# Kernel optimization log

Measured on AMD Instinct MI355X. Metric: run time of the kernel, lower is better.

The kernel has to match this reference:

```python
import jax, jax.numpy as jnp
import numpy as np

D_K = 32  # hard-coded in original module


def setup_inputs() -> dict:
    key = jax.random.key(0)
    kq, kk, kv, km = jax.random.split(key, 4)
    B, H, S, D = 4, 12, 2048, D_K
    Q = jax.random.normal(kq, (B, H, S, D), dtype=jnp.float32)
    K = jax.random.normal(kk, (B, H, S, D), dtype=jnp.float32)
    V = jax.random.normal(kv, (B, H, S, D), dtype=jnp.float32)
    attn_mask = jax.random.bernoulli(km, 0.5, (B, H, S, S))
    return {"Q": Q, "K": K, "V": V, "attn_mask": attn_mask}


def tanh_max(a):
    # (exp(a) - exp(-a)) / sum_over_keys(exp(a) + exp(-a))
    ea = jnp.exp(a)
    ena = jnp.exp(-a)
    return (ea - ena) / (ea + ena).sum(axis=-1, keepdims=True)


def reference(Q, K, V, attn_mask):
    # scores: [B,H,S,S]
    scores = jnp.einsum("bhqd,bhkd->bhqk", Q, K) / np.sqrt(D_K).astype(np.float32)
    attn = tanh_max(scores)
    # NOTE: original calls attn.masked_fill(attn_mask, 0.0) WITHOUT assignment
    # (non-in-place), so the mask has no effect. Reproduced faithfully.
    context = jnp.einsum("bhqk,bhkd->bhqd", attn, V)
    return context
```

## Files before the change

### kernel.cpp

```cpp
#include <hip/hip_runtime.h>
#include <hip/hip_bf16.h>
#include <cstdint>
#include <cstddef>


#define SLEN 2048
#define DK   32
#define NBH  48
#define NCH  64
#define PROW 36

typedef __attribute__((ext_vector_type(8))) short bf16x8;
typedef __attribute__((ext_vector_type(4))) float f32x4;
typedef const __attribute__((address_space(1))) void* gas_ptr;
typedef __attribute__((address_space(3))) void*       las_ptr;

__device__ __forceinline__ unsigned pk2(float a, float b) {
    __hip_bfloat162 h = __float22bfloat162_rn(make_float2(a, b));
    union { __hip_bfloat162 h2; unsigned u; } cv; cv.h2 = h; return cv.u;
}
__device__ __forceinline__ unsigned short f2b(float x) {
    __hip_bfloat16 h = __float2bfloat16(x);
    union { __hip_bfloat16 h; unsigned short u; } cv; cv.h = h; return cv.u;
}

__global__ __launch_bounds__(256, 3)
void attn_fused(const float* __restrict__ Q, const float* __restrict__ K,
                const float* __restrict__ V, float* __restrict__ Out) {
    __shared__ __align__(16) float          Kst[2][32 * 32];
    __shared__ __align__(16) unsigned short Vst[2][32 * PROW];

    const int tid  = threadIdx.x;
    const int lane = tid & 63;
    const int wv   = tid >> 6;
    const int quad = lane >> 4;
    const int l16  = lane & 15;

    const int b   = blockIdx.x;
    const int xcd = b & 7;
    const int i   = b >> 3;
    const int bh  = xcd * 6 + (i % 6);
    const int qblk = i / 6;
    const int qbase = qblk * 128 + wv * 32;

    const float sc = 0.17677669529663687f * 1.4426950408889634f;
    union { bf16x8 v; unsigned u[4]; } aQ0, aQ1;
    {
        const float* qp0 = Q + ((size_t)bh * SLEN + qbase + l16) * DK + quad * 8;
        float4 qa = *(const float4*)qp0;
        float4 qb = *(const float4*)(qp0 + 4);
        aQ0.u[0] = pk2(qa.x * sc, qa.y * sc); aQ0.u[1] = pk2(qa.z * sc, qa.w * sc);
        aQ0.u[2] = pk2(qb.x * sc, qb.y * sc); aQ0.u[3] = pk2(qb.z * sc, qb.w * sc);
        const float* qp1 = qp0 + 16 * DK;
        float4 qc = *(const float4*)qp1;
        float4 qd = *(const float4*)(qp1 + 4);
        aQ1.u[0] = pk2(qc.x * sc, qc.y * sc); aQ1.u[1] = pk2(qc.z * sc, qc.w * sc);
        aQ1.u[2] = pk2(qd.x * sc, qd.y * sc); aQ1.u[3] = pk2(qd.z * sc, qd.w * sc);
    }

    const float* Kh = K + (size_t)bh * SLEN * DK;
    const float* Vh = V + (size_t)bh * SLEN * DK;

    const int grow   = wv * 8 + (lane >> 3);
    const int spos   = lane & 7;
    const int schunk = spos ^ ((grow >> 1) & 7);
    const int ksrc   = grow * 32 + schunk * 4;
    const int vsrc   = grow * 32 + spos * 4;
    const int vcol   = spos * 4;

    const int rkey0 = 8 * (l16 >> 2) + 2 * (l16 & 3);
    const int rxor  = (rkey0 >> 1) & 7;
    const int rc0   = ((2 * quad + 0) ^ rxor) * 4;
    const int rc1   = ((2 * quad + 1) ^ rxor) * 4;

    f32x4 o00 = {0,0,0,0}, o01 = {0,0,0,0};
    f32x4 o10 = {0,0,0,0}, o11 = {0,0,0,0};
    float den0 = 0.f, den1 = 0.f;
    const f32x4 zero = {0,0,0,0};

    __builtin_amdgcn_global_load_lds((gas_ptr)(Kh + ksrc),
                                     (las_ptr)(&Kst[0][wv * 256]), 16, 0, 0);
    float4 vreg = *(const float4*)(Vh + vsrc);
    {
        unsigned short* vtw = &Vst[0][0];
        vtw[(vcol + 0) * PROW + grow] = f2b(vreg.x);
        vtw[(vcol + 1) * PROW + grow] = f2b(vreg.y);
        vtw[(vcol + 2) * PROW + grow] = f2b(vreg.z);
        vtw[(vcol + 3) * PROW + grow] = f2b(vreg.w);
    }
    __syncthreads();

    for (int c = 0; c < NCH; ++c) {
        const int buf = c & 1, nbuf = buf ^ 1;
        if (c + 1 < NCH) {
            __builtin_amdgcn_global_load_lds(
                (gas_ptr)(Kh + (c + 1) * 1024 + ksrc),
                (las_ptr)(&Kst[nbuf][wv * 256]), 16, 0, 0);
            vreg = *(const float4*)(Vh + (c + 1) * 1024 + vsrc);
        }

        const float* kb_ = &Kst[buf][0];
        float4 e0 = *(const float4*)(kb_ + rkey0 * 32 + rc0);
        float4 e1 = *(const float4*)(kb_ + rkey0 * 32 + rc1);
        float4 d0 = *(const float4*)(kb_ + (rkey0 + 1) * 32 + rc0);
        float4 d1 = *(const float4*)(kb_ + (rkey0 + 1) * 32 + rc1);
        union { bf16x8 v; unsigned u[4]; } kf0, kf1;
        kf0.u[0] = pk2(e0.x, e0.y); kf0.u[1] = pk2(e0.z, e0.w);
        kf0.u[2] = pk2(e1.x, e1.y); kf0.u[3] = pk2(e1.z, e1.w);
        kf1.u[0] = pk2(d0.x, d0.y); kf1.u[1] = pk2(d0.z, d0.w);
        kf1.u[2] = pk2(d1.x, d1.y); kf1.u[3] = pk2(d1.z, d1.w);

        f32x4 s00 = __builtin_amdgcn_mfma_f32_16x16x32_bf16(kf0.v, aQ0.v, zero, 0, 0, 0);
        f32x4 s01 = __builtin_amdgcn_mfma_f32_16x16x32_bf16(kf1.v, aQ0.v, zero, 0, 0, 0);
        f32x4 s10 = __builtin_amdgcn_mfma_f32_16x16x32_bf16(kf0.v, aQ1.v, zero, 0, 0, 0);
        f32x4 s11 = __builtin_amdgcn_mfma_f32_16x16x32_bf16(kf1.v, aQ1.v, zero, 0, 0, 0);

        const unsigned short* vt = &Vst[buf][0];
        union { bf16x8 v; uint2 h[2]; } V0, V1;
        {
            const unsigned short* p0 = vt + l16 * PROW + quad * 8;
            V0.h[0] = *(const uint2*)p0;
            V0.h[1] = *(const uint2*)(p0 + 4);
            const unsigned short* p1 = vt + (16 + l16) * PROW + quad * 8;
            V1.h[0] = *(const uint2*)p1;
            V1.h[1] = *(const uint2*)(p1 + 4);
        }

        union { bf16x8 v; unsigned u[4]; } aP0, aP1;
        #pragma unroll
        for (int r = 0; r < 4; ++r) {
            float e0_  = __builtin_amdgcn_exp2f(s00[r]);
            float en0_ = __builtin_amdgcn_exp2f(-s00[r]);
            float e1_  = __builtin_amdgcn_exp2f(s01[r]);
            float en1_ = __builtin_amdgcn_exp2f(-s01[r]);
            den0 += (e0_ + en0_) + (e1_ + en1_);
            aP0.u[r] = pk2(e0_ - en0_, e1_ - en1_);
        }
        #pragma unroll
        for (int r = 0; r < 4; ++r) {
            float e0_  = __builtin_amdgcn_exp2f(s10[r]);
            float en0_ = __builtin_amdgcn_exp2f(-s10[r]);
            float e1_  = __builtin_amdgcn_exp2f(s11[r]);
            float en1_ = __builtin_amdgcn_exp2f(-s11[r]);
            den1 += (e0_ + en0_) + (e1_ + en1_);
            aP1.u[r] = pk2(e0_ - en0_, e1_ - en1_);
        }

        o00 = __builtin_amdgcn_mfma_f32_16x16x32_bf16(aP0.v, V0.v, o00, 0, 0, 0);
        o01 = __builtin_amdgcn_mfma_f32_16x16x32_bf16(aP0.v, V1.v, o01, 0, 0, 0);
        o10 = __builtin_amdgcn_mfma_f32_16x16x32_bf16(aP1.v, V0.v, o10, 0, 0, 0);
        o11 = __builtin_amdgcn_mfma_f32_16x16x32_bf16(aP1.v, V1.v, o11, 0, 0, 0);

        if (c + 1 < NCH) {
            unsigned short* vtw = &Vst[nbuf][0];
            vtw[(vcol + 0) * PROW + grow] = f2b(vreg.x);
            vtw[(vcol + 1) * PROW + grow] = f2b(vreg.y);
            vtw[(vcol + 2) * PROW + grow] = f2b(vreg.z);
            vtw[(vcol + 3) * PROW + grow] = f2b(vreg.w);
        }
        __syncthreads();
    }

    den0 += __shfl_xor(den0, 16); den0 += __shfl_xor(den0, 32);
    den1 += __shfl_xor(den1, 16); den1 += __shfl_xor(den1, 32);

    float* outp = Out + ((size_t)bh * SLEN + qbase) * DK;
    #pragma unroll
    for (int rr = 0; rr < 4; ++rr) {
        float inv0 = 1.0f / __shfl(den0, quad * 4 + rr, 16);
        float inv1 = 1.0f / __shfl(den1, quad * 4 + rr, 16);
        int q0 = quad * 4 + rr;
        int q1 = 16 + quad * 4 + rr;
        outp[(size_t)q0 * DK + l16]      = o00[rr] * inv0;
        outp[(size_t)q0 * DK + 16 + l16] = o01[rr] * inv0;
        outp[(size_t)q1 * DK + l16]      = o10[rr] * inv1;
        outp[(size_t)q1 * DK + 16 + l16] = o11[rr] * inv1;
    }
}

extern "C" void kernel_launch(void* const* d_in, const int* in_sizes, int n_in,
                              void* d_out, int out_size, void* d_ws, size_t ws_size,
                              hipStream_t stream) {
    const float* Q = (const float*)d_in[0];
    const float* K = (const float*)d_in[1];
    const float* V = (const float*)d_in[2];
    float* Out = (float*)d_out;
    attn_fused<<<dim3(NBH * 16), dim3(256), 0, stream>>>(Q, K, V, Out);
}
```

Before: 956.5 us.

## Load K directly into registers and give each wave private V staging without block barriers

The shared K staging through LDS (global_load_lds) is removed. Each lane now loads its K fragment straight from global memory into registers, prefetching one chunk ahead. V staging becomes per-wave, double-buffered and written as packed bf16 pairs, which lets all __syncthreads calls in the loop go away. The cost is that each wave now reads all of K and V from global/L2 itself instead of sharing one block-wide load, which is four times the redundant traffic. Register pressure also rises from the prefetch registers, and a per-wave LDS buffer is reused with no intra-wave barrier, which relies on wave-level lockstep ordering.

```diff
diff --git a/kernel.cpp b/kernel.cpp
--- a/kernel.cpp
+++ b/kernel.cpp
@@ -8,27 +8,20 @@
 #define DK   32
 #define NBH  48
 #define NCH  64
-#define PROW 36
+#define VROW 36
 
 typedef __attribute__((ext_vector_type(8))) short bf16x8;
 typedef __attribute__((ext_vector_type(4))) float f32x4;
-typedef const __attribute__((address_space(1))) void* gas_ptr;
-typedef __attribute__((address_space(3))) void*       las_ptr;
 
 __device__ __forceinline__ unsigned pk2(float a, float b) {
     __hip_bfloat162 h = __float22bfloat162_rn(make_float2(a, b));
     union { __hip_bfloat162 h2; unsigned u; } cv; cv.h2 = h; return cv.u;
 }
-__device__ __forceinline__ unsigned short f2b(float x) {
-    __hip_bfloat16 h = __float2bfloat16(x);
-    union { __hip_bfloat16 h; unsigned short u; } cv; cv.h = h; return cv.u;
-}
 
 __global__ __launch_bounds__(256, 3)
 void attn_fused(const float* __restrict__ Q, const float* __restrict__ K,
                 const float* __restrict__ V, float* __restrict__ Out) {
-    __shared__ __align__(16) float          Kst[2][32 * 32];
-    __shared__ __align__(16) unsigned short Vst[2][32 * PROW];
+    __shared__ __align__(16) unsigned short Vst[4][2][32 * VROW];
 
     const int tid  = threadIdx.x;
     const int lane = tid & 63;
@@ -36,10 +29,10 @@
     const int quad = lane >> 4;
     const int l16  = lane & 15;
 
-    const int b   = blockIdx.x;
-    const int xcd = b & 7;
-    const int i   = b >> 3;
-    const int bh  = xcd * 6 + (i % 6);
+    const int b    = blockIdx.x;
+    const int xcd  = b & 7;
+    const int i    = b >> 3;
+    const int bh   = xcd * 6 + (i % 6);
     const int qblk = i / 6;
     const int qbase = qblk * 128 + wv * 32;
 
@@ -61,90 +54,96 @@
     const float* Kh = K + (size_t)bh * SLEN * DK;
     const float* Vh = V + (size_t)bh * SLEN * DK;
 
-    const int grow   = wv * 8 + (lane >> 3);
-    const int spos   = lane & 7;
-    const int schunk = spos ^ ((grow >> 1) & 7);
-    const int ksrc   = grow * 32 + schunk * 4;
-    const int vsrc   = grow * 32 + spos * 4;
-    const int vcol   = spos * 4;
+    const int keyl = 8 * (l16 >> 2) + 2 * (l16 & 3);
+    const float* kp = Kh + (size_t)keyl * DK + quad * 8;
 
-    const int rkey0 = 8 * (l16 >> 2) + 2 * (l16 & 3);
-    const int rxor  = (rkey0 >> 1) & 7;
-    const int rc0   = ((2 * quad + 0) ^ rxor) * 4;
-    const int rc1   = ((2 * quad + 1) ^ rxor) * 4;
+    const int vr = lane >> 3;
+    const int vc = lane & 7;
+    const float* vp = Vh + (size_t)(2 * vr) * DK + vc * 4;
 
     f32x4 o00 = {0,0,0,0}, o01 = {0,0,0,0};
     f32x4 o10 = {0,0,0,0}, o11 = {0,0,0,0};
     float den0 = 0.f, den1 = 0.f;
     const f32x4 zero = {0,0,0,0};
 
-    __builtin_amdgcn_global_load_lds((gas_ptr)(Kh + ksrc),
-                                     (las_ptr)(&Kst[0][wv * 256]), 16, 0, 0);
-    float4 vreg = *(const float4*)(Vh + vsrc);
+    unsigned*             Vw = (unsigned*)&Vst[wv][0][0];
+    const unsigned short* Vr = &Vst[wv][0][0];
+
+    float4 ka0 = *(const float4*)(kp);
+    float4 ka1 = *(const float4*)(kp + 4);
+    float4 kb0 = *(const float4*)(kp + DK);
+    float4 kb1 = *(const float4*)(kp + DK + 4);
     {
-        unsigned short* vtw = &Vst[0][0];
-        vtw[(vcol + 0) * PROW + grow] = f2b(vreg.x);
-        vtw[(vcol + 1) * PROW + grow] = f2b(vreg.y);
-        vtw[(vcol + 2) * PROW + grow] = f2b(vreg.z);
-        vtw[(vcol + 3) * PROW + grow] = f2b(vreg.w);
+        float4 va0 = *(const float4*)(vp);
+        float4 vb0 = *(const float4*)(vp + DK);
+        float4 va1 = *(const float4*)(vp + 16 * DK);
+        float4 vb1 = *(const float4*)(vp + 17 * DK);
+        Vw[(4*vc + 0) * 18 + vr]     = pk2(va0.x, vb0.x);
+        Vw[(4*vc + 1) * 18 + vr]     = pk2(va0.y, vb0.y);
+        Vw[(4*vc + 2) * 18 + vr]     = pk2(va0.z, vb0.z);
+        Vw[(4*vc + 3) * 18 + vr]     = pk2(va0.w, vb0.w);
+        Vw[(4*vc + 0) * 18 + 8 + vr] = pk2(va1.x, vb1.x);
+        Vw[(4*vc + 1) * 18 + 8 + vr] = pk2(va1.y, vb1.y);
+        Vw[(4*vc + 2) * 18 + 8 + vr] = pk2(va1.z, vb1.z);
+        Vw[(4*vc + 3) * 18 + 8 + vr] = pk2(va1.w, vb1.w);
     }
-    __syncthreads();
 
+    #pragma unroll 2
     for (int c = 0; c < NCH; ++c) {
-        const int buf = c & 1, nbuf = buf ^ 1;
+        const int buf  = c & 1;
+        const int nbuf = buf ^ 1;
+
+        float4 nka0, nka1, nkb0, nkb1, nva0, nvb0, nva1, nvb1;
         if (c + 1 < NCH) {
-            __builtin_amdgcn_global_load_lds(
-                (gas_ptr)(Kh + (c + 1) * 1024 + ksrc),
-                (las_ptr)(&Kst[nbuf][wv * 256]), 16, 0, 0);
-            vreg = *(const float4*)(Vh + (c + 1) * 1024 + vsrc);
+            const float* kc = kp + (size_t)(c + 1) * 1024;
+            nka0 = *(const float4*)(kc);
+            nka1 = *(const float4*)(kc + 4);
+            nkb0 = *(const float4*)(kc + DK);
+            nkb1 = *(const float4*)(kc + DK + 4);
+            const float* vcp = vp + (size_t)(c + 1) * 1024;
+            nva0 = *(const float4*)(vcp);
+            nvb0 = *(const float4*)(vcp + DK);
+            nva1 = *(const float4*)(vcp + 16 * DK);
+            nvb1 = *(const float4*)(vcp + 17 * DK);
         }
 
-        const float* kb_ = &Kst[buf][0];
-        float4 e0 = *(const float4*)(kb_ + rkey0 * 32 + rc0);
-        float4 e1 = *(const float4*)(kb_ + rkey0 * 32 + rc1);
-        float4 d0 = *(const float4*)(kb_ + (rkey0 + 1) * 32 + rc0);
-        float4 d1 = *(const float4*)(kb_ + (rkey0 + 1) * 32 + rc1);
         union { bf16x8 v; unsigned u[4]; } kf0, kf1;
-        kf0.u[0] = pk2(e0.x, e0.y); kf0.u[1] = pk2(e0.z, e0.w);
-        kf0.u[2] = pk2(e1.x, e1.y); kf0.u[3] = pk2(e1.z, e1.w);
-        kf1.u[0] = pk2(d0.x, d0.y); kf1.u[1] = pk2(d0.z, d0.w);
-        kf1.u[2] = pk2(d1.x, d1.y); kf1.u[3] = pk2(d1.z, d1.w);
+        kf0.u[0] = pk2(ka0.x, ka0.y); kf0.u[1] = pk2(ka0.z, ka0.w);
+        kf0.u[2] = pk2(ka1.x, ka1.y); kf0.u[3] = pk2(ka1.z, ka1.w);
+        kf1.u[0] = pk2(kb0.x, kb0.y); kf1.u[1] = pk2(kb0.z, kb0.w);
+        kf1.u[2] = pk2(kb1.x, kb1.y); kf1.u[3] = pk2(kb1.z, kb1.w);
 
         f32x4 s00 = __builtin_amdgcn_mfma_f32_16x16x32_bf16(kf0.v, aQ0.v, zero, 0, 0, 0);
         f32x4 s01 = __builtin_amdgcn_mfma_f32_16x16x32_bf16(kf1.v, aQ0.v, zero, 0, 0, 0);
         f32x4 s10 = __builtin_amdgcn_mfma_f32_16x16x32_bf16(kf0.v, aQ1.v, zero, 0, 0, 0);
         f32x4 s11 = __builtin_amdgcn_mfma_f32_16x16x32_bf16(kf1.v, aQ1.v, zero, 0, 0, 0);
 
-        const unsigned short* vt = &Vst[buf][0];
-        union { bf16x8 v; uint2 h[2]; } V0, V1;
-        {
-            const unsigned short* p0 = vt + l16 * PROW + quad * 8;
-            V0.h[0] = *(const uint2*)p0;
-            V0.h[1] = *(const uint2*)(p0 + 4);
-            const unsigned short* p1 = vt + (16 + l16) * PROW + quad * 8;
-            V1.h[0] = *(const uint2*)p1;
-            V1.h[1] = *(const uint2*)(p1 + 4);
-        }
-
         union { bf16x8 v; unsigned u[4]; } aP0, aP1;
         #pragma unroll
         for (int r = 0; r < 4; ++r) {
-            float e0_  = __builtin_amdgcn_exp2f(s00[r]);
-            float en0_ = __builtin_amdgcn_exp2f(-s00[r]);
-            float e1_  = __builtin_amdgcn_exp2f(s01[r]);
-            float en1_ = __builtin_amdgcn_exp2f(-s01[r]);
-            den0 += (e0_ + en0_) + (e1_ + en1_);
-            aP0.u[r] = pk2(e0_ - en0_, e1_ - en1_);
+            float e0  = __builtin_amdgcn_exp2f(s00[r]);
+            float en0 = __builtin_amdgcn_exp2f(-s00[r]);
+            float e1  = __builtin_amdgcn_exp2f(s01[r]);
+            float en1 = __builtin_amdgcn_exp2f(-s01[r]);
+            den0 += (e0 + en0) + (e1 + en1);
+            aP0.u[r] = pk2(e0 - en0, e1 - en1);
         }
         #pragma unroll
         for (int r = 0; r < 4; ++r) {
-            float e0_  = __builtin_amdgcn_exp2f(s10[r]);
-            float en0_ = __builtin_amdgcn_exp2f(-s10[r]);
-            float e1_  = __builtin_amdgcn_exp2f(s11[r]);
-            float en1_ = __builtin_amdgcn_exp2f(-s11[r]);
-            den1 += (e0_ + en0_) + (e1_ + en1_);
-            aP1.u[r] = pk2(e0_ - en0_, e1_ - en1_);
+            float e0  = __builtin_amdgcn_exp2f(s10[r]);
+            float en0 = __builtin_amdgcn_exp2f(-s10[r]);
+            float e1  = __builtin_amdgcn_exp2f(s11[r]);
+            float en1 = __builtin_amdgcn_exp2f(-s11[r]);
+            den1 += (e0 + en0) + (e1 + en1);
+            aP1.u[r] = pk2(e0 - en0, e1 - en1);
         }
+
+        const unsigned short* vt = Vr + buf * (32 * VROW);
+        union { bf16x8 v; uint2 h[2]; } V0, V1;
+        V0.h[0] = *(const uint2*)(vt + VROW * l16 + 8 * quad);
+        V0.h[1] = *(const uint2*)(vt + VROW * l16 + 8 * quad + 4);
+        V1.h[0] = *(const uint2*)(vt + VROW * (16 + l16) + 8 * quad);
+        V1.h[1] = *(const uint2*)(vt + VROW * (16 + l16) + 8 * quad + 4);
 
         o00 = __builtin_amdgcn_mfma_f32_16x16x32_bf16(aP0.v, V0.v, o00, 0, 0, 0);
         o01 = __builtin_amdgcn_mfma_f32_16x16x32_bf16(aP0.v, V1.v, o01, 0, 0, 0);
@@ -152,13 +151,17 @@
         o11 = __builtin_amdgcn_mfma_f32_16x16x32_bf16(aP1.v, V1.v, o11, 0, 0, 0);
 
         if (c + 1 < NCH) {
-            unsigned short* vtw = &Vst[nbuf][0];
-            vtw[(vcol + 0) * PROW + grow] = f2b(vreg.x);
-            vtw[(vcol + 1) * PROW + grow] = f2b(vreg.y);
-            vtw[(vcol + 2) * PROW + grow] = f2b(vreg.z);
-            vtw[(vcol + 3) * PROW + grow] = f2b(vreg.w);
+            unsigned* vw = Vw + nbuf * (32 * 18);
+            vw[(4*vc + 0) * 18 + vr]     = pk2(nva0.x, nvb0.x);
+            vw[(4*vc + 1) * 18 + vr]     = pk2(nva0.y, nvb0.y);
+            vw[(4*vc + 2) * 18 + vr]     = pk2(nva0.z, nvb0.z);
+            vw[(4*vc + 3) * 18 + vr]     = pk2(nva0.w, nvb0.w);
+            vw[(4*vc + 0) * 18 + 8 + vr] = pk2(nva1.x, nvb1.x);
+            vw[(4*vc + 1) * 18 + 8 + vr] = pk2(nva1.y, nvb1.y);
+            vw[(4*vc + 2) * 18 + 8 + vr] = pk2(nva1.z, nvb1.z);
+            vw[(4*vc + 3) * 18 + 8 + vr] = pk2(nva1.w, nvb1.w);
+            ka0 = nka0; ka1 = nka1; kb0 = nkb0; kb1 = nkb1;
         }
-        __syncthreads();
     }
 
     den0 += __shfl_xor(den0, 16); den0 += __shfl_xor(den0, 32);
```

New measurement: 978.9 us. 1.02x slower.
